# Kernel tuning notes

Hardware: AMD Instinct MI355X
Metric: run time of the kernel (lower is better)

The kernel has to match this reference:

```python
import jax, jax.numpy as jnp
import numpy as np

M = 48      # number of MPS components / Fourier modes
L = 48      # num_site
N = 256     # batch of samples
PI = float(np.pi)


def setup_inputs() -> dict:
    key = jax.random.key(0)
    k1, k2, k3, k4 = jax.random.split(key, 4)
    inp = jax.random.uniform(k1, (N, L), jnp.float32)
    theta = 0.01 * jax.random.uniform(k2, (L, M), jnp.float32, minval=-PI / 2, maxval=PI / 2)
    coef = 1.0 + 0.01 * jax.random.uniform(k3, (M,), jnp.float32, minval=-1.0, maxval=1.0)
    rand_u = jax.random.uniform(k4, (L, N), jnp.float32)
    return {"inp": inp, "theta": theta, "coef": coef, "rand_u": rand_u}


def _output_mps(inp, theta, coef):
    # fourier encoding: angle (N,M,L) = inp (N,L) * m*pi/2
    m_vals = jnp.arange(1, M + 1, dtype=inp.dtype)
    angle = inp[:, None, :] * (m_vals * (PI / 2))[None, :, None]
    emb = jnp.stack([jnp.cos(angle), jnp.sin(angle)], axis=-1)  # (N,M,L,2)
    c, s = jnp.cos(theta), jnp.sin(theta)                        # (L,M)
    R = jnp.stack([jnp.stack([c, -s], axis=-1), jnp.stack([s, c], axis=-1)], axis=-2)  # (L,M,2,2)
    mpo = jnp.transpose(R, (1, 0, 2, 3))                         # (M,L,2,2)
    return jnp.einsum('m,mlpq,nmlq->nmlp', coef, mpo, emb)       # (N,M,L,2)


def _inner(mps):
    # vmapped inner_product: sum_{m,k} prod_l <mps[m,l], mps[k,l]>
    t = jnp.einsum('nmlp,nklp->nmkl', mps, mps)  # (N,M,M,L)
    return jnp.sum(jnp.prod(t, axis=-1), axis=(1, 2))  # (N,)


def _zipper(mps, rand_u):
    # Incremental form of zipper_MPS: zeroing the (1-bit) component at each
    # re-cloning + re-masking the full prefix every step (same math).
    e0 = jnp.array([1.0, 0.0], mps.dtype)  # zeroes component 0 (bit=1 branch)
    e1 = jnp.array([0.0, 1.0], mps.dtype)  # zeroes component 1 (bit=0 branch)
    pos = jnp.arange(L)

    def step(mps_cur, xs):
        l, u = xs
        oh = (pos == l).astype(mps_cur.dtype)                     # (L,) one-hot at site l
        denom = jnp.abs(_inner(mps_cur))                           # marginal_prob(prefix)
        mps1 = mps_cur * (1.0 - oh[None, None, :, None] * e0)     # assume bit=1 at l
        p1 = jnp.abs(_inner(mps1)) / denom
        bit = (u < p1).astype(jnp.int32)                           # (N,)
        mps0 = mps_cur * (1.0 - oh[None, None, :, None] * e1)     # bit=0 branch
        mps_new = jnp.where((bit == 1)[:, None, None, None], mps1, mps0)
        return mps_new, bit

    mps_final, bits = jax.lax.scan(step, mps, (pos, rand_u))
    measurement = bits.T                                           # (N,L) int32
    P_m = jnp.abs(_inner(mps_final)) / jnp.abs(_inner(mps))        # normalized prob
    return measurement, P_m


def reference(inp, theta, coef, rand_u):
    mps = _output_mps(inp, theta, coef)
    return _zipper(mps, rand_u)
```

## Files before the change

### kernel.cpp

```cpp
#include <hip/hip_runtime.h>
#include <math.h>

#define M_ 48
#define L_ 48
#define N_ 256
#define THREADS 256
#define NWAVE (THREADS/64)
#define NPAIR_UT 1176
#define PPT 5

__launch_bounds__(THREADS, 1)
__global__ void mps_sample_kernel(const float* __restrict__ inp,
                                  const float* __restrict__ theta,
                                  const float* __restrict__ coef,
                                  const float* __restrict__ rand_u,
                                  float* __restrict__ out)
{
    const int n   = blockIdx.x;
    const int tid = threadIdx.x;

    __shared__ double s_pxy[L_][M_][2];
    __shared__ double s_part[2][4][NWAVE];
    __shared__ float  s_u[L_];

    const double PI_2 = 1.5707963267948966;

    #pragma unroll
    for (int i = 0; i < 9; ++i) {
        int j = tid + THREADS * i;
        int l = j / M_, m = j - l * M_;
        double a  = (double)inp[n * L_ + l] * ((double)(m + 1) * PI_2);
        double th = (double)theta[l * M_ + m];
        double sv, cv; sincos(th + a, &sv, &cv);
        double cf = (double)coef[m];
        s_pxy[l][m][0] = cf * cv;
        s_pxy[l][m][1] = cf * sv;
    }
    if (tid < L_) s_u[tid] = rand_u[tid * N_ + n];

    int pm[PPT], pk[PPT];
    double wgt[PPT];
    #pragma unroll
    for (int i = 0; i < PPT; ++i) {
        int p = tid + THREADS * i;
        if (p < NPAIR_UT) {
            int m = 0, r = p;
            while (r >= M_ - m) { r -= M_ - m; ++m; }
            pm[i] = m; pk[i] = m + r;
            wgt[i] = (r == 0) ? 1.0 : 2.0;
        } else { pm[i] = 0; pk[i] = 0; wgt[i] = 0.0; }
    }
    __syncthreads();

    double ckpt[5][PPT];
    {
        double C[PPT];
        #pragma unroll
        for (int i = 0; i < PPT; ++i) C[i] = wgt[i];
        #pragma unroll
        for (int s = 4; s >= 0; --s) {
            #pragma unroll
            for (int lp = 7; lp >= 0; --lp) {
                int l = 8 * (s + 1) + lp;
                #pragma unroll
                for (int i = 0; i < PPT; ++i) {
                    double2 vm = *(const double2*)&s_pxy[l][pm[i]][0];
                    double2 vk = *(const double2*)&s_pxy[l][pk[i]][0];
                    C[i] *= vm.x * vk.x + vm.y * vk.y;
                }
            }
            #pragma unroll
            for (int i = 0; i < PPT; ++i) ckpt[s][i] = C[i];
        }
    }

    double G[PPT];
    #pragma unroll
    for (int i = 0; i < PPT; ++i) G[i] = 1.0;

    double denom = 0.0, initd = 1.0;
    float  myBit = 0.0f;

    #pragma unroll
    for (int seg = 0; seg < 6; ++seg) {
        double X[8][PPT], Y[8][PPT];
        #pragma unroll
        for (int j = 0; j < 8; ++j) {
            int l2 = 8 * seg + j;
            #pragma unroll
            for (int i = 0; i < PPT; ++i) {
                double2 vm = *(const double2*)&s_pxy[l2][pm[i]][0];
                double2 vk = *(const double2*)&s_pxy[l2][pk[i]][0];
                X[j][i] = vm.x * vk.x;
                Y[j][i] = vm.y * vk.y;
            }
        }
        double R[8][PPT];
        #pragma unroll
        for (int i = 0; i < PPT; ++i)
            R[7][i] = (seg == 5) ? wgt[i] : ckpt[seg == 5 ? 0 : seg][i];
        #pragma unroll
        for (int j = 6; j >= 0; --j)
            #pragma unroll
            for (int i = 0; i < PPT; ++i)
                R[j][i] = R[j + 1][i] * (X[j + 1][i] + Y[j + 1][i]);

        #pragma unroll
        for (int half = 0; half < 4; ++half) {
            const int ls  = 2 * half;
            const int l   = 8 * seg + ls;
            const int par = half & 1;
            double n1L = 0.0, h0 = 0.0, h1 = 0.0, nT = 0.0;
            #pragma unroll
            for (int i = 0; i < PPT; ++i) {
                double t0 = G[i] * R[ls][i];
                double t1 = G[i] * R[ls + 1][i];
                n1L = fma(t0, Y[ls][i], n1L);
                if (seg == 0 && half == 0) nT = fma(t0, X[0][i], nT);
                h0 = fma(t1 * X[ls][i], Y[ls + 1][i], h0);
                h1 = fma(t1 * Y[ls][i], Y[ls + 1][i], h1);
            }
            #pragma unroll
            for (int off = 1; off < 64; off <<= 1) {
                n1L += __shfl_xor(n1L, off, 64);
                h0  += __shfl_xor(h0,  off, 64);
                h1  += __shfl_xor(h1,  off, 64);
                if (seg == 0 && half == 0) nT += __shfl_xor(nT, off, 64);
            }
            const int wv = tid >> 6;
            if ((tid & 63) == 0) {
                s_part[par][0][wv] = n1L; s_part[par][1][wv] = h0;
                s_part[par][2][wv] = h1;
                if (seg == 0 && half == 0) s_part[par][3][wv] = nT;
            }
            __syncthreads();
            double2 a0 = *(const double2*)&s_part[par][0][0];
            double2 b0 = *(const double2*)&s_part[par][0][2];
            double2 a1 = *(const double2*)&s_part[par][1][0];
            double2 b1 = *(const double2*)&s_part[par][1][2];
            double2 a2 = *(const double2*)&s_part[par][2][0];
            double2 b2 = *(const double2*)&s_part[par][2][2];
            double sn1 = (a0.x + a0.y) + (b0.x + b0.y);
            double sh0 = (a1.x + a1.y) + (b1.x + b1.y);
            double sh1 = (a2.x + a2.y) + (b2.x + b2.y);
            if (seg == 0 && half == 0) {
                double2 a3 = *(const double2*)&s_part[par][3][0];
                double2 b3 = *(const double2*)&s_part[par][3][2];
                double snT = (a3.x + a3.y) + (b3.x + b3.y);
                denom = fabs(snT + sn1);
                initd = denom;
            }
            double v1 = fabs(sn1);
            int bitA   = ((double)s_u[l] * denom < v1) ? 1 : 0;
            denom      = bitA ? v1 : fabs(denom - sn1);
            double n1b = bitA ? sh1 : sh0;
            double v2  = fabs(n1b);
            int bitB   = ((double)s_u[l + 1] * denom < v2) ? 1 : 0;
            denom      = bitB ? v2 : fabs(denom - n1b);
            #pragma unroll
            for (int i = 0; i < PPT; ++i) {
                double c0 = bitA ? Y[ls][i]     : X[ls][i];
                double c1 = bitB ? Y[ls + 1][i] : X[ls + 1][i];
                G[i] *= c0 * c1;
            }
            if (tid == l)     myBit = (float)bitA;
            if (tid == l + 1) myBit = (float)bitB;
        }
    }

    if (tid < L_)  out[n * L_ + tid] = myBit;
    if (tid == 0)  out[N_ * L_ + n] = (float)(denom / initd);
}

extern "C" void kernel_launch(void* const* d_in, const int* in_sizes, int n_in,
                              void* d_out, int out_size, void* d_ws, size_t ws_size,
                              hipStream_t stream) {
    const float* inp    = (const float*)d_in[0];
    const float* theta  = (const float*)d_in[1];
    const float* coef   = (const float*)d_in[2];
    const float* rand_u = (const float*)d_in[3];
    float* out = (float*)d_out;
    mps_sample_kernel<<<N_, THREADS, 0, stream>>>(inp, theta, coef, rand_u, out);
}
```

Measured before the change: 95.31 us.

## Use per-thread contiguous pair chunks and DPP wave reductions

Reassigns the upper-triangular (m,k) pairs so that each thread owns one row index m and five consecutive k values, taken from a compile-time table. This lets the s_pxy[l][m] load be hoisted out of the per-pair loop, cutting LDS reads. The table orders slots by the low bits of k, presumably to spread LDS banks. It also replaces the shuffle-xor butterfly with a DPP row-shift/broadcast reduction whose total lands in lane 63. The remapping changes the floating-point summation order, and correctness depends on the table covering every pair exactly once.

```diff
diff --git a/kernel.cpp b/kernel.cpp
--- a/kernel.cpp
+++ b/kernel.cpp
@@ -5,9 +5,48 @@
 #define L_ 48
 #define N_ 256
 #define THREADS 256
-#define NWAVE (THREADS/64)
-#define NPAIR_UT 1176
+#define NWAVE 4
 #define PPT 5
+
+struct ChunkTab { short cm[256]; short ck0[256]; };
+constexpr ChunkTab make_tab() {
+    ChunkTab t{};
+    int bsz[8] = {};
+    for (int m = 0; m < 48; ++m)
+        for (int j = 0; 5 * j < 48 - m; ++j) bsz[(m + 5 * j) & 7]++;
+    int slot = 0;
+    for (int r = 0; r < 48; ++r)
+        for (int b = 0; b < 8; ++b)
+            if (bsz[b] > r) {
+                int cnt = 0;
+                for (int m = 0; m < 48; ++m)
+                    for (int j = 0; 5 * j < 48 - m; ++j)
+                        if (((m + 5 * j) & 7) == b) {
+                            if (cnt == r) { t.cm[slot] = (short)m; t.ck0[slot] = (short)(m + 5 * j); }
+                            ++cnt;
+                        }
+                ++slot;
+            }
+    for (; slot < 256; ++slot) { t.cm[slot] = 0; t.ck0[slot] = 127; }
+    return t;
+}
+__device__ constexpr ChunkTab g_tab = make_tab();
+
+template<int CTRL, int RMASK>
+__device__ __forceinline__ double dpp_add(double v) {
+    int lo = __builtin_amdgcn_update_dpp(0, __double2loint(v), CTRL, RMASK, 0xf, true);
+    int hi = __builtin_amdgcn_update_dpp(0, __double2hiint(v), CTRL, RMASK, 0xf, true);
+    return v + __hiloint2double(hi, lo);
+}
+__device__ __forceinline__ double wave_sum63(double v) {
+    v = dpp_add<0x111, 0xf>(v);
+    v = dpp_add<0x112, 0xf>(v);
+    v = dpp_add<0x114, 0xf>(v);
+    v = dpp_add<0x118, 0xf>(v);
+    v = dpp_add<0x142, 0xa>(v);
+    v = dpp_add<0x143, 0xc>(v);
+    return v;
+}
 
 __launch_bounds__(THREADS, 1)
 __global__ void mps_sample_kernel(const float* __restrict__ inp,
@@ -38,17 +77,14 @@
     }
     if (tid < L_) s_u[tid] = rand_u[tid * N_ + n];
 
-    int pm[PPT], pk[PPT];
-    double wgt[PPT];
+    const int cm = g_tab.cm[tid];
+    const int k0 = g_tab.ck0[tid];
+    int pk[PPT]; double wgt[PPT];
     #pragma unroll
     for (int i = 0; i < PPT; ++i) {
-        int p = tid + THREADS * i;
-        if (p < NPAIR_UT) {
-            int m = 0, r = p;
-            while (r >= M_ - m) { r -= M_ - m; ++m; }
-            pm[i] = m; pk[i] = m + r;
-            wgt[i] = (r == 0) ? 1.0 : 2.0;
-        } else { pm[i] = 0; pk[i] = 0; wgt[i] = 0.0; }
+        int k = k0 + i;
+        wgt[i] = (k > 47) ? 0.0 : ((k == cm) ? 1.0 : 2.0);
+        pk[i]  = (k > 47) ? 47 : k;
     }
     __syncthreads();
 
@@ -62,9 +98,9 @@
             #pragma unroll
             for (int lp = 7; lp >= 0; --lp) {
                 int l = 8 * (s + 1) + lp;
+                double2 vm = *(const double2*)&s_pxy[l][cm][0];
                 #pragma unroll
                 for (int i = 0; i < PPT; ++i) {
-                    double2 vm = *(const double2*)&s_pxy[l][pm[i]][0];
                     double2 vk = *(const double2*)&s_pxy[l][pk[i]][0];
                     C[i] *= vm.x * vk.x + vm.y * vk.y;
                 }
@@ -87,9 +123,9 @@
         #pragma unroll
         for (int j = 0; j < 8; ++j) {
             int l2 = 8 * seg + j;
+            double2 vm = *(const double2*)&s_pxy[l2][cm][0];
             #pragma unroll
             for (int i = 0; i < PPT; ++i) {
-                double2 vm = *(const double2*)&s_pxy[l2][pm[i]][0];
                 double2 vk = *(const double2*)&s_pxy[l2][pk[i]][0];
                 X[j][i] = vm.x * vk.x;
                 Y[j][i] = vm.y * vk.y;
@@ -120,15 +156,12 @@
                 h0 = fma(t1 * X[ls][i], Y[ls + 1][i], h0);
                 h1 = fma(t1 * Y[ls][i], Y[ls + 1][i], h1);
             }
-            #pragma unroll
-            for (int off = 1; off < 64; off <<= 1) {
-                n1L += __shfl_xor(n1L, off, 64);
-                h0  += __shfl_xor(h0,  off, 64);
-                h1  += __shfl_xor(h1,  off, 64);
-                if (seg == 0 && half == 0) nT += __shfl_xor(nT, off, 64);
-            }
-            const int wv = tid >> 6;
-            if ((tid & 63) == 0) {
+            n1L = wave_sum63(n1L);
+            h0  = wave_sum63(h0);
+            h1  = wave_sum63(h1);
+            if (seg == 0 && half == 0) nT = wave_sum63(nT);
+            if ((tid & 63) == 63) {
+                const int wv = tid >> 6;
                 s_part[par][0][wv] = n1L; s_part[par][1][wv] = h0;
                 s_part[par][2][wv] = h1;
                 if (seg == 0 && half == 0) s_part[par][3][wv] = nT;
```

After: 82.40 us (median of 2 runs). 13.6% less time.
